# Kernel tuning notes

Hardware: AMD Instinct MI355X
Metric: run time of the kernel (lower is better)

The kernel has to match this reference:

```python
import jax, jax.numpy as jnp
import numpy as np

L, D, H, F, E, K = 2, 512, 8, 2048, 8, 2
V, B, S, T, PAD = 32000, 2, 1024, 1024, 0


def _pe(n, d):
    pos = jnp.arange(n, dtype=jnp.float32)[:, None]
    div = jnp.exp(jnp.arange(0, d, 2, dtype=jnp.float32) * (-np.log(10000.0) / d))
    pe = jnp.zeros((n, d), jnp.float32)
    pe = pe.at[:, 0::2].set(jnp.sin(pos * div)).at[:, 1::2].set(jnp.cos(pos * div))
    return pe


def _ln(x, g, b):
    m = x.mean(-1, keepdims=True)
    v = ((x - m) ** 2).mean(-1, keepdims=True)
    return (x - m) / jnp.sqrt(v + 1e-5) * g + b


def _mha(q_in, k_in, v_in, w, b, mask):
    # w: [4,D,D] (q,k,v,out), b: [4,D]; mask broadcastable to [B,H,Sq,Sk] (True=keep)
    Bq, Sq, Dm = q_in.shape
    Sk = k_in.shape[1]
    dk = Dm // H
    q = (q_in @ w[0] + b[0]).reshape(Bq, Sq, H, dk).transpose(0, 2, 1, 3)
    k = (k_in @ w[1] + b[1]).reshape(Bq, Sk, H, dk).transpose(0, 2, 1, 3)
    v = (v_in @ w[2] + b[2]).reshape(Bq, Sk, H, dk).transpose(0, 2, 1, 3)
    s = jnp.einsum('bhqd,bhkd->bhqk', q, k) / np.sqrt(dk).astype(np.float32)
    s = jnp.where(mask, s, jnp.float32(-1e9))
    a = jax.nn.softmax(s, axis=-1)
    c = jnp.einsum('bhqk,bhkd->bhqd', a, v).transpose(0, 2, 1, 3).reshape(Bq, Sq, Dm)
    return c @ w[3] + b[3]


def _moe(x, gw, gb, w1, b1, w2, b2):
    # token-choice top-k routing with softmax gate probs (no renormalization)
    Bx, Sx, Dm = x.shape
    N = Bx * Sx
    xf = x.reshape(N, Dm)
    probs = jax.nn.softmax(xf @ gw + gb, axis=-1)              # [N,E]
    topv, topi = jax.lax.top_k(probs, K)                        # [N,K]
    comb = jnp.zeros_like(probs).at[jnp.arange(N)[:, None], topi].set(topv)  # [N,E] sparse combine weights
    h = jax.nn.relu(jnp.einsum('nd,edf->nef', xf, w1) + b1)     # [N,E,F]
    eo = jnp.einsum('nef,efd->ned', h, w2) + b2                 # [N,E,D]
    y = jnp.einsum('ne,ned->nd', comb, eo)
    return y.reshape(Bx, Sx, Dm)


def setup_inputs():
    key = jax.random.key(0)
    ks = iter(jax.random.split(key, 32))
    sd, sf = 1.0 / np.sqrt(D), 1.0 / np.sqrt(F)

    def nrm(shape, scale):
        return jax.random.normal(next(ks), shape, jnp.float32) * np.float32(scale)

    inp = {}
    inp['src'] = jax.random.randint(next(ks), (B, S), 0, V)
    inp['tgt'] = jax.random.randint(next(ks), (B, T), 0, V)
    inp['enc_emb'] = nrm((V, D), 0.02).at[PAD].set(0.0)
    inp['dec_emb'] = nrm((V, D), 0.02).at[PAD].set(0.0)
    inp['enc_attn_w'] = nrm((L, 4, D, D), sd)
    inp['enc_attn_b'] = jnp.zeros((L, 4, D), jnp.float32)
    inp['enc_ln_g'] = jnp.ones((L, 2, D), jnp.float32)
    inp['enc_ln_b'] = jnp.zeros((L, 2, D), jnp.float32)
    inp['enc_gate_w'] = nrm((L, D, E), sd)
    inp['enc_gate_b'] = jnp.zeros((L, E), jnp.float32)
    inp['enc_w1'] = nrm((L, E, D, F), sd)
    inp['enc_b1'] = jnp.zeros((L, E, F), jnp.float32)
    inp['enc_w2'] = nrm((L, E, F, D), sf)
    inp['enc_b2'] = jnp.zeros((L, E, D), jnp.float32)
    inp['dec_sa_w'] = nrm((L, 4, D, D), sd)
    inp['dec_sa_b'] = jnp.zeros((L, 4, D), jnp.float32)
    inp['dec_ca_w'] = nrm((L, 4, D, D), sd)
    inp['dec_ca_b'] = jnp.zeros((L, 4, D), jnp.float32)
    inp['dec_ln_g'] = jnp.ones((L, 3, D), jnp.float32)
    inp['dec_ln_b'] = jnp.zeros((L, 3, D), jnp.float32)
    inp['dec_gate_w'] = nrm((L, D, E), sd)
    inp['dec_gate_b'] = jnp.zeros((L, E), jnp.float32)
    inp['dec_w1'] = nrm((L, E, D, F), sd)
    inp['dec_b1'] = jnp.zeros((L, E, F), jnp.float32)
    inp['dec_w2'] = nrm((L, E, F, D), sf)
    inp['dec_b2'] = jnp.zeros((L, E, D), jnp.float32)
    inp['out_w'] = nrm((D, V), sd)
    inp['out_b'] = jnp.zeros((V,), jnp.float32)
    return inp


def reference(src, tgt, enc_emb, dec_emb, enc_attn_w, enc_attn_b, enc_ln_g, enc_ln_b,
              enc_gate_w, enc_gate_b, enc_w1, enc_b1, enc_w2, enc_b2,
              dec_sa_w, dec_sa_b, dec_ca_w, dec_ca_b, dec_ln_g, dec_ln_b,
              dec_gate_w, dec_gate_b, dec_w1, dec_b1, dec_w2, dec_b2, out_w, out_b):
    src_mask = (src != PAD)[:, None, None, :]                                  # [B,1,1,S]
    causal = jnp.tril(jnp.ones((T, T), bool))
    tgt_mask = (tgt != PAD)[:, None, None, :] & causal[None, None]             # [B,1,T,T]

    x = enc_emb[src] + _pe(S, D)[None]                                         # dropout = identity (eval)
    for l in range(L):
        a = _mha(x, x, x, enc_attn_w[l], enc_attn_b[l], src_mask)
        x = _ln(x + a, enc_ln_g[l, 0], enc_ln_b[l, 0])
        f = _moe(x, enc_gate_w[l], enc_gate_b[l], enc_w1[l], enc_b1[l], enc_w2[l], enc_b2[l])
        x = _ln(x + f, enc_ln_g[l, 1], enc_ln_b[l, 1])
    enc_out = x

    y = dec_emb[tgt] + _pe(T, D)[None]
    for l in range(L):
        a = _mha(y, y, y, dec_sa_w[l], dec_sa_b[l], tgt_mask)
        y = _ln(y + a, dec_ln_g[l, 0], dec_ln_b[l, 0])
        c = _mha(y, enc_out, enc_out, dec_ca_w[l], dec_ca_b[l], src_mask)
        y = _ln(y + c, dec_ln_g[l, 1], dec_ln_b[l, 1])
        f = _moe(y, dec_gate_w[l], dec_gate_b[l], dec_w1[l], dec_b1[l], dec_w2[l], dec_b2[l])
        y = _ln(y + f, dec_ln_g[l, 2], dec_ln_b[l, 2])

    return y @ out_w + out_b                                                    # [B,T,V]
```

## Files before the change

### kernel.cpp

```cpp
#include <hip/hip_runtime.h>
#include <hip/hip_bf16.h>

#define L_ 2
#define D_ 512
#define H_ 8
#define DK_ 64
#define F_ 2048
#define E_ 8
#define V_ 32000
#define B_ 2
#define S_ 1024
#define T_ 1024
#define NTOK (B_*S_)
#define MAXPAD 4608
#define RB64   72
#define QLD 1536

typedef unsigned short u16;
typedef _Float16 f16x8 __attribute__((ext_vector_type(8)));
typedef _Float16 f16x4 __attribute__((ext_vector_type(4)));
typedef float f32x4 __attribute__((ext_vector_type(4)));

__device__ __forceinline__ void gload16(const void* g, const void* l) {
    __builtin_amdgcn_global_load_lds(
        (const __attribute__((address_space(1))) void*)g,
        (__attribute__((address_space(3))) void*)l, 16, 0, 0);
}

__device__ __forceinline__ void split_f16(float v, _Float16& h, _Float16& l) {
    h = (_Float16)v;
    l = (_Float16)(v - (float)h);
}

__global__ __launch_bounds__(256) void embed_pe(const int* __restrict__ toks,
                                                const float* __restrict__ emb,
                                                _Float16* __restrict__ oh,
                                                _Float16* __restrict__ ol, int Slen)
{
    int n = blockIdx.x;
    int spos = n % Slen;
    int tok = toks[n];
    const float* erow = emb + (size_t)tok * D_;
    size_t rb = (size_t)n * D_;
    for (int j = threadIdx.x; j < D_; j += 256) {
        int i = j >> 1;
        float arg = (float)spos * expf(-(float)i * 0.035977892f);
        float pe = (j & 1) ? cosf(arg) : sinf(arg);
        float v = erow[j] + pe;
        _Float16 h, l; split_f16(v, h, l);
        oh[rb + j] = h; ol[rb + j] = l;
    }
}

template<bool WLO>
__global__ __launch_bounds__(256) void transpose_w(const float* __restrict__ in,
                                                   _Float16* __restrict__ oh,
                                                   _Float16* __restrict__ ol, int R, int C)
{
    __shared__ float t[64][65];
    size_t sb = (size_t)blockIdx.z * R * C;
    in += sb; oh += sb; if (WLO) ol += sb;
    int c0 = blockIdx.x * 64, r0 = blockIdx.y * 64;
    int tid = threadIdx.x;
    {
        int r = tid >> 4;
        int cq = (tid & 15) * 4;
        #pragma unroll
        for (int p = 0; p < 4; ++p) {
            int rr = r + p * 16;
            float4 v = *(const float4*)&in[(size_t)(r0 + rr) * C + c0 + cq];
            t[rr][cq] = v.x; t[rr][cq + 1] = v.y; t[rr][cq + 2] = v.z; t[rr][cq + 3] = v.w;
        }
    }
    __syncthreads();
    int rp = (tid & 15) * 4;
    int cb = tid >> 4;
    #pragma unroll
    for (int p = 0; p < 4; ++p) {
        int c = cb + p * 16;
        f16x4 hv, lv;
        #pragma unroll
        for (int j = 0; j < 4; ++j) {
            float v = t[rp + j][c];
            _Float16 h = (_Float16)v;
            hv[j] = h;
            if (WLO) lv[j] = (_Float16)(v - (float)h);
        }
        *(f16x4*)&oh[(size_t)(c0 + c) * R + r0 + rp] = hv;
        if (WLO) *(f16x4*)&ol[(size_t)(c0 + c) * R + r0 + rp] = lv;
    }
}

template<int MODE, bool RELU, int OUTMODE, int PASSES, int TM, int TN>
__global__ __launch_bounds__(256, 2) void gemm_mfma(
    const _Float16* __restrict__ Ah, const _Float16* __restrict__ Al,
    const _Float16* __restrict__ Wh, const _Float16* __restrict__ Wl,
    const float* __restrict__ biasbase,
    float* __restrict__ Cf, _Float16* __restrict__ Ch, _Float16* __restrict__ Cl,
    _Float16* __restrict__ vt_h, _Float16* __restrict__ vt_l, int cbase,
    int M, int Kd, int N, int ldc,
    const int* __restrict__ route_tok, const int* __restrict__ rb_expert,
    const int* __restrict__ pad_base, const int* __restrict__ counts)
{
    constexpr int AR = TM / 32;
    constexpr int BR = TN / 32;
    int row0 = blockIdx.x * TM;
    const _Float16* Wmh = Wh;
    const _Float16* Wml = Wl;
    const float* bias = biasbase;
    int vend = M;
    if (MODE != 0) {
        int total = pad_base[E_];
        if (row0 >= total) return;
        int e = rb_expert[row0 >> 6];
        vend = pad_base[e] + counts[e];
        Wmh = Wh + (size_t)e * Kd * N;
        if (PASSES == 3) Wml = Wl + (size_t)e * Kd * N;
        bias = biasbase + (size_t)e * N;
    }
    int col0 = blockIdx.y * TN;
    int tid = threadIdx.x;
    int lane = tid & 63, w = tid >> 6;
    int wm = w >> 1, wn = w & 1;

    __shared__ _Float16 lds[(PASSES == 3 ? 2 : 1) * (TM + TN) * 64];
    _Float16* lAh = lds;
    _Float16* lBh = lds + TM * 64;
    _Float16* lAl = (PASSES == 3) ? lds + (TM + TN) * 64 : nullptr;
    _Float16* lBl = (PASSES == 3) ? lds + (TM + TN) * 64 + TM * 64 : nullptr;

    int srow8 = lane >> 3;
    int q8 = lane & 7;
    size_t aoff[AR], boff[BR];
    #pragma unroll
    for (int j = 0; j < AR; ++j) {
        int m = w * (TM / 4) + j * 8 + srow8;
        int gr = row0 + m;
        int ar = (MODE == 1) ? route_tok[gr] : gr;
        int ss = (q8 ^ (m & 7)) << 3;
        aoff[j] = (size_t)ar * Kd + ss;
    }
    #pragma unroll
    for (int j = 0; j < BR; ++j) {
        int m = w * (TN / 4) + j * 8 + srow8;
        int ss = (q8 ^ (m & 7)) << 3;
        boff[j] = (size_t)(col0 + m) * Kd + ss;
    }

    f32x4 zero4 = {0.f, 0.f, 0.f, 0.f};
    f32x4 acc[AR][BR];
    #pragma unroll
    for (int i = 0; i < AR; ++i)
        #pragma unroll
        for (int j = 0; j < BR; ++j) acc[i][j] = zero4;

    int lm = lane & 15, kg = lane >> 4;

    for (int k0 = 0; k0 < Kd; k0 += 64) {
        #pragma unroll
        for (int j = 0; j < AR; ++j) {
            int lb = (w * (TM / 4) + j * 8) * 64;
            gload16(Ah + aoff[j] + k0, lAh + lb);
            if (PASSES == 3) gload16(Al + aoff[j] + k0, lAl + lb);
        }
        #pragma unroll
        for (int j = 0; j < BR; ++j) {
            int lb = (w * (TN / 4) + j * 8) * 64;
            gload16(Wmh + boff[j] + k0, lBh + lb);
            if (PASSES == 3) gload16(Wml + boff[j] + k0, lBl + lb);
        }
        __syncthreads();
        #pragma unroll
        for (int ks = 0; ks < 2; ++ks) {
            f16x8 ah[AR], bh[BR];
            #pragma unroll
            for (int i = 0; i < AR; ++i) {
                int m = wm * (TM / 2) + i * 16 + lm;
                ah[i] = *(const f16x8*)&lAh[m * 64 + ((((ks << 2) + kg) ^ (m & 7)) << 3)];
            }
            #pragma unroll
            for (int j = 0; j < BR; ++j) {
                int n = wn * (TN / 2) + j * 16 + lm;
                bh[j] = *(const f16x8*)&lBh[n * 64 + ((((ks << 2) + kg) ^ (n & 7)) << 3)];
            }
            #pragma unroll
            for (int i = 0; i < AR; ++i)
                #pragma unroll
                for (int jn = 0; jn < BR; ++jn)
                    acc[i][jn] = __builtin_amdgcn_mfma_f32_16x16x32_f16(ah[i], bh[jn], acc[i][jn], 0, 0, 0);
            if (PASSES == 3) {
                f16x8 bl[BR];
                #pragma unroll
                for (int j = 0; j < BR; ++j) {
                    int n = wn * (TN / 2) + j * 16 + lm;
                    bl[j] = *(const f16x8*)&lBl[n * 64 + ((((ks << 2) + kg) ^ (n & 7)) << 3)];
                }
                #pragma unroll
                for (int i = 0; i < AR; ++i)
                    #pragma unroll
                    for (int jn = 0; jn < BR; ++jn)
                        acc[i][jn] = __builtin_amdgcn_mfma_f32_16x16x32_f16(ah[i], bl[jn], acc[i][jn], 0, 0, 0);
                f16x8 al[AR];
                #pragma unroll
                for (int i = 0; i < AR; ++i) {
                    int m = wm * (TM / 2) + i * 16 + lm;
                    al[i] = *(const f16x8*)&lAl[m * 64 + ((((ks << 2) + kg) ^ (m & 7)) << 3)];
                }
                #pragma unroll
                for (int i = 0; i < AR; ++i)
                    #pragma unroll
                    for (int jn = 0; jn < BR; ++jn)
                        acc[i][jn] = __builtin_amdgcn_mfma_f32_16x16x32_f16(al[i], bh[jn], acc[i][jn], 0, 0, 0);
            }
        }
        __syncthreads();
    }

    float bv[BR];
    #pragma unroll
    for (int jn = 0; jn < BR; ++jn) bv[jn] = bias[col0 + wn * (TN / 2) + jn * 16 + lm];
    int rowb = row0 + wm * (TM / 2) + (lane >> 4) * 4;

    if (OUTMODE == 2 && (col0 + cbase) >= 1024) {
        #pragma unroll
        for (int i = 0; i < AR; ++i) {
            int row = rowb + i * 16;
            int b = row >> 10, q = row & 1023;
            #pragma unroll
            for (int jn = 0; jn < BR; ++jn) {
                int vcol = col0 + cbase - 1024 + wn * (TN / 2) + jn * 16 + lm;
                int hh = vcol >> 6, dd = vcol & 63;
                f16x4 hv, lv;
                #pragma unroll
                for (int r = 0; r < 4; ++r) {
                    float v = acc[i][jn][r] + bv[jn];
                    _Float16 x1, x2; split_f16(v, x1, x2);
                    hv[r] = x1; lv[r] = x2;
                }
                size_t vtoff = ((size_t)((b << 3) + hh) * 64 + dd) * 1024 + q;
                *(f16x4*)&vt_h[vtoff] = hv;
                *(f16x4*)&vt_l[vtoff] = lv;
            }
        }
        return;
    }

    #pragma unroll
    for (int i = 0; i < AR; ++i) {
        #pragma unroll
        for (int r = 0; r < 4; ++r) {
            int row = rowb + i * 16 + r;
            if (MODE != 0 && row >= vend) continue;
            #pragma unroll
            for (int jn = 0; jn < BR; ++jn) {
                float v = acc[i][jn][r] + bv[jn];
                if (RELU) v = fmaxf(v, 0.f);
                int c = col0 + wn * (TN / 2) + jn * 16 + lm;
                if (OUTMODE == 0) {
                    Cf[(size_t)row * ldc + c] = v;
                } else {
                    _Float16 h, l; split_f16(v, h, l);
                    Ch[(size_t)row * ldc + cbase + c] = h;
                    Cl[(size_t)row * ldc + cbase + c] = l;
                }
            }
        }
    }
}

template<int CAUSAL>
__global__ __launch_bounds__(512, 1) void attn_flash(
    const _Float16* __restrict__ qkvh, const _Float16* __restrict__ qkvl,
    const _Float16* __restrict__ vth, const _Float16* __restrict__ vtl,
    const int* __restrict__ ktoks,
    _Float16* __restrict__ ch, _Float16* __restrict__ cl)
{
    int q0 = blockIdx.x * 64;
    int bh = blockIdx.y, b = bh >> 3, h = bh & 7;
    int tid = threadIdx.x, lane = tid & 63, w = tid >> 6;
    int qg = w & 3, kh = w >> 2;
    int lm = lane & 15, kg = lane >> 4;
    int srow8 = lane >> 3, q8 = lane & 7;
    int tb = b * S_;

    __shared__ _Float16 smem[49152];
    _Float16* hb  = smem + kh * 16384;
    _Float16* lKh = hb;
    _Float16* lKl = hb + 4096;
    _Float16* lVh = hb + 8192;
    _Float16* lVl = hb + 12288;
    _Float16* lPh = smem + 32768 + w * 1024;
    _Float16* lPl = smem + 40960 + w * 1024;

    size_t qbase = (size_t)b * S_ * QLD + h * DK_;
    const _Float16* Qh = qkvh + qbase;
    const _Float16* Ql = qkvl + qbase;
    const _Float16* Kh = qkvh + qbase + 512;
    const _Float16* Kl = qkvl + qbase + 512;
    const _Float16* Vh = vth + (size_t)bh * 64 * 1024;
    const _Float16* Vl = vtl + (size_t)bh * 64 * 1024;

    f16x8 qfh[2], qfl[2];
    {
        int qr = q0 + qg * 16 + lm;
        #pragma unroll
        for (int ks = 0; ks < 2; ++ks) {
            qfh[ks] = *(const f16x8*)&Qh[(size_t)qr * QLD + ks * 32 + kg * 8];
            qfl[ks] = *(const f16x8*)&Ql[(size_t)qr * QLD + ks * 32 + kg * 8];
        }
    }

    float mreg[4], lreg[4];
    f32x4 od[4];
    f32x4 zero4 = {0.f, 0.f, 0.f, 0.f};
    #pragma unroll
    for (int r = 0; r < 4; ++r) { mreg[r] = -1e30f; lreg[r] = 0.f; }
    #pragma unroll
    for (int jn = 0; jn < 4; ++jn) od[jn] = zero4;

    int qrow[4];
    #pragma unroll
    for (int r = 0; r < 4; ++r) qrow[r] = q0 + qg * 16 + (lane >> 4) * 4 + r;

    int nkt = CAUSAL ? (q0 >> 6) + 1 : 16;
    int nhalf = (nkt + 1) >> 1;

    for (int it = 0; it < nhalf; ++it) {
        int kt = 2 * it + kh;
        bool active = kt < nkt;
        int k0 = kt * 64;

        if (active) {
            #pragma unroll
            for (int j = 0; j < 2; ++j) {
                int row = qg * 16 + j * 8 + srow8;
                int lb = (qg * 16 + j * 8) * 64;
                int ss = (q8 ^ (row & 7)) << 3;
                gload16(Kh + (size_t)(k0 + row) * QLD + ss, lKh + lb);
                gload16(Kl + (size_t)(k0 + row) * QLD + ss, lKl + lb);
                gload16(Vh + (size_t)row * 1024 + k0 + ss, lVh + lb);
                gload16(Vl + (size_t)row * 1024 + k0 + ss, lVl + lb);
            }
        }
        __syncthreads();

        if (active) {
            bool diag = CAUSAL && (kt == (q0 >> 6));
            f32x4 accs[4];
            #pragma unroll
            for (int jn = 0; jn < 4; ++jn) accs[jn] = zero4;
            #pragma unroll
            for (int ks = 0; ks < 2; ++ks) {
                #pragma unroll
                for (int jn = 0; jn < 4; ++jn) {
                    int n = jn * 16 + lm;
                    int koff = n * 64 + ((((ks << 2) + kg) ^ (n & 7)) << 3);
                    f16x8 bhv = *(const f16x8*)&lKh[koff];
                    f16x8 blv = *(const f16x8*)&lKl[koff];
                    accs[jn] = __builtin_amdgcn_mfma_f32_16x16x32_f16(qfh[ks], bhv, accs[jn], 0, 0, 0);
                    accs[jn] = __builtin_amdgcn_mfma_f32_16x16x32_f16(qfh[ks], blv, accs[jn], 0, 0, 0);
                    accs[jn] = __builtin_amdgcn_mfma_f32_16x16x32_f16(qfl[ks], bhv, accs[jn], 0, 0, 0);
                }
            }

            float sv[4][4];
            #pragma unroll
            for (int jn = 0; jn < 4; ++jn) {
                int kglob = k0 + jn * 16 + lm;
                bool pad_ok = (ktoks[tb + kglob] != 0);
                #pragma unroll
                for (int r = 0; r < 4; ++r) {
                    float s = accs[jn][r] * 0.125f;
                    bool keep = pad_ok && (!diag || kglob <= qrow[r]);
                    sv[jn][r] = keep ? s : -1e9f;
                }
            }
            float pv[4][4];
            #pragma unroll
            for (int r = 0; r < 4; ++r) {
                float tm = fmaxf(fmaxf(sv[0][r], sv[1][r]), fmaxf(sv[2][r], sv[3][r]));
                tm = fmaxf(tm, __shfl_xor(tm, 1));
                tm = fmaxf(tm, __shfl_xor(tm, 2));
                tm = fmaxf(tm, __shfl_xor(tm, 4));
                tm = fmaxf(tm, __shfl_xor(tm, 8));
                float mnew = fmaxf(mreg[r], tm);
                float corr = expf(mreg[r] - mnew);
                lreg[r] *= corr;
                #pragma unroll
                for (int jn = 0; jn < 4; ++jn) od[jn][r] *= corr;
                float psum = 0.f;
                #pragma unroll
                for (int jn = 0; jn < 4; ++jn) {
                    float p = expf(sv[jn][r] - mnew);
                    pv[jn][r] = p;
                    psum += p;
                }
                psum += __shfl_xor(psum, 1);
                psum += __shfl_xor(psum, 2);
                psum += __shfl_xor(psum, 4);
                psum += __shfl_xor(psum, 8);
                lreg[r] += psum;
                mreg[r] = mnew;
            }

            #pragma unroll
            for (int jn = 0; jn < 4; ++jn) {
                int col = jn * 16 + lm;
                #pragma unroll
                for (int r = 0; r < 4; ++r) {
                    int rr = (lane >> 4) * 4 + r;
                    int idx = rr * 64 + (((col >> 3) ^ (rr & 7)) << 3) + (col & 7);
                    _Float16 hh, ll; split_f16(pv[jn][r], hh, ll);
                    lPh[idx] = hh; lPl[idx] = ll;
                }
            }

            #pragma unroll
            for (int ks = 0; ks < 2; ++ks) {
                int poff = lm * 64 + ((((ks << 2) + kg) ^ (lm & 7)) << 3);
                f16x8 pah = *(const f16x8*)&lPh[poff];
                f16x8 pal = *(const f16x8*)&lPl[poff];
                #pragma unroll
                for (int jn = 0; jn < 4; ++jn) {
                    int n = jn * 16 + lm;
                    int noff = n * 64 + ((((ks << 2) + kg) ^ (n & 7)) << 3);
                    f16x8 vbh = *(const f16x8*)&lVh[noff];
                    f16x8 vbl = *(const f16x8*)&lVl[noff];
                    od[jn] = __builtin_amdgcn_mfma_f32_16x16x32_f16(pah, vbh, od[jn], 0, 0, 0);
                    od[jn] = __builtin_amdgcn_mfma_f32_16x16x32_f16(pah, vbl, od[jn], 0, 0, 0);
                    od[jn] = __builtin_amdgcn_mfma_f32_16x16x32_f16(pal, vbh, od[jn], 0, 0, 0);
                }
            }
        }
        __syncthreads();
    }

    float* mrg = (float*)(smem + 32768);
    if (kh == 1) {
        float* mp = mrg + ((size_t)qg * 64 + lane) * 24;
        #pragma unroll
        for (int jn = 0; jn < 4; ++jn)
            #pragma unroll
            for (int r = 0; r < 4; ++r) mp[jn * 4 + r] = od[jn][r];
        #pragma unroll
        for (int r = 0; r < 4; ++r) { mp[16 + r] = mreg[r]; mp[20 + r] = lreg[r]; }
    }
    __syncthreads();
    if (kh == 0) {
        float* mp = mrg + ((size_t)qg * 64 + lane) * 24;
        #pragma unroll
        for (int r = 0; r < 4; ++r) {
            float m1 = mp[16 + r], l1 = mp[20 + r];
            float m = fmaxf(mreg[r], m1);
            float c0 = expf(mreg[r] - m), c1 = expf(m1 - m);
            float inv = 1.0f / (lreg[r] * c0 + l1 * c1);
            size_t rbase = (size_t)(tb + qrow[r]) * D_ + h * DK_;
            #pragma unroll
            for (int jn = 0; jn < 4; ++jn) {
                float o = (od[jn][r] * c0 + mp[jn * 4 + r] * c1) * inv;
                _Float16 hh, ll; split_f16(o, hh, ll);
                int d = jn * 16 + lm;
                ch[rbase + d] = hh; cl[rbase + d] = ll;
            }
        }
    }
}

template<bool GATE>
__global__ __launch_bounds__(256) void ln_add(const _Float16* __restrict__ xh,
                                              const _Float16* __restrict__ xl,
                                              const float* __restrict__ r,
                                              const float* __restrict__ g,
                                              const float* __restrict__ be,
                                              _Float16* __restrict__ oh,
                                              _Float16* __restrict__ ol,
                                              const float* __restrict__ gw,
                                              const float* __restrict__ gb,
                                              float* __restrict__ lg)
{
    int row = blockIdx.x;
    size_t rb = (size_t)row * D_;
    int tid = threadIdx.x;
    float v0 = (float)xh[rb + tid] + (float)xl[rb + tid] + r[rb + tid];
    float v1 = (float)xh[rb + tid + 256] + (float)xl[rb + tid + 256] + r[rb + tid + 256];
    float s = v0 + v1;
    for (int off = 32; off; off >>= 1) s += __shfl_down(s, off);
    __shared__ float red[8];
    __shared__ float gred[4][E_];
    int lane = tid & 63, wid = tid >> 6;
    if (!lane) red[wid] = s;
    __syncthreads();
    if (!tid) red[4] = (red[0] + red[1] + red[2] + red[3]) * (1.0f / 512.0f);
    __syncthreads();
    float m = red[4];
    float d0 = v0 - m, d1 = v1 - m;
    s = d0 * d0 + d1 * d1;
    for (int off = 32; off; off >>= 1) s += __shfl_down(s, off);
    if (!lane) red[wid] = s;
    __syncthreads();
    if (!tid) red[5] = rsqrtf((red[0] + red[1] + red[2] + red[3]) * (1.0f / 512.0f) + 1e-5f);
    __syncthreads();
    float rstd = red[5];
    float y0 = d0 * rstd * g[tid] + be[tid];
    float y1 = d1 * rstd * g[tid + 256] + be[tid + 256];
    _Float16 h, l;
    split_f16(y0, h, l); oh[rb + tid] = h; ol[rb + tid] = l;
    split_f16(y1, h, l); oh[rb + tid + 256] = h; ol[rb + tid + 256] = l;
    if (GATE) {
        float acc[E_];
        const float* g0 = gw + (size_t)tid * E_;
        const float* g1 = gw + (size_t)(tid + 256) * E_;
        #pragma unroll
        for (int e = 0; e < E_; ++e) acc[e] = y0 * g0[e] + y1 * g1[e];
        #pragma unroll
        for (int e = 0; e < E_; ++e)
            for (int off = 32; off; off >>= 1) acc[e] += __shfl_down(acc[e], off);
        if (!lane) {
            #pragma unroll
            for (int e = 0; e < E_; ++e) gred[wid][e] = acc[e];
        }
        __syncthreads();
        if (tid < E_)
            lg[(size_t)row * E_ + tid] = gred[0][tid] + gred[1][tid] + gred[2][tid] + gred[3][tid] + gb[tid];
    }
}

__global__ __launch_bounds__(256) void ln_add_moe(const _Float16* __restrict__ xh,
                                                  const _Float16* __restrict__ xl,
                                                  const float* __restrict__ eo,
                                                  const float* __restrict__ topv,
                                                  const int* __restrict__ route_row,
                                                  const float* __restrict__ g,
                                                  const float* __restrict__ be,
                                                  _Float16* __restrict__ oh,
                                                  _Float16* __restrict__ ol)
{
    int row = blockIdx.x;
    int r0 = route_row[row * 2], r1 = route_row[row * 2 + 1];
    float w0 = topv[row * 2], w1 = topv[row * 2 + 1];
    size_t rb = (size_t)row * D_;
    const float* e0 = eo + (size_t)r0 * D_;
    const float* e1 = eo + (size_t)r1 * D_;
    int tid = threadIdx.x;
    float v0 = (float)xh[rb + tid] + (float)xl[rb + tid] + w0 * e0[tid] + w1 * e1[tid];
    float v1 = (float)xh[rb + tid + 256] + (float)xl[rb + tid + 256] + w0 * e0[tid + 256] + w1 * e1[tid + 256];
    float s = v0 + v1;
    for (int off = 32; off; off >>= 1) s += __shfl_down(s, off);
    __shared__ float red[8];
    int lane = tid & 63, wid = tid >> 6;
    if (!lane) red[wid] = s;
    __syncthreads();
    if (!tid) red[4] = (red[0] + red[1] + red[2] + red[3]) * (1.0f / 512.0f);
    __syncthreads();
    float m = red[4];
    float d0 = v0 - m, d1 = v1 - m;
    s = d0 * d0 + d1 * d1;
    for (int off = 32; off; off >>= 1) s += __shfl_down(s, off);
    if (!lane) red[wid] = s;
    __syncthreads();
    if (!tid) red[5] = rsqrtf((red[0] + red[1] + red[2] + red[3]) * (1.0f / 512.0f) + 1e-5f);
    __syncthreads();
    float rstd = red[5];
    float y0 = d0 * rstd * g[tid] + be[tid];
    float y1 = d1 * rstd * g[tid + 256] + be[tid + 256];
    _Float16 h, l;
    split_f16(y0, h, l); oh[rb + tid] = h; ol[rb + tid] = l;
    split_f16(y1, h, l); oh[rb + tid + 256] = h; ol[rb + tid + 256] = l;
}

__global__ __launch_bounds__(1024) void gate_top2_routes(const float* __restrict__ lg,
                                                         float* __restrict__ topv,
                                                         int* __restrict__ route_tok,
                                                         int* __restrict__ route_row,
                                                         int* __restrict__ counts,
                                                         int* __restrict__ pad_base,
                                                         int* __restrict__ rb_expert)
{
    __shared__ int eid[NTOK * 2];
    __shared__ unsigned short chist[256][8];
    __shared__ int pb[E_ + 1];
    __shared__ int cnt[E_];
    int t = threadIdx.x;
    #pragma unroll
    for (int s2 = 0; s2 < 2; ++s2) {
        int n = t * 2 + s2;
        float l0[E_], p[E_];
        float m = -1e30f;
        #pragma unroll
        for (int e = 0; e < E_; ++e) { l0[e] = lg[n * E_ + e]; m = fmaxf(m, l0[e]); }
        float su = 0.f;
        #pragma unroll
        for (int e = 0; e < E_; ++e) { p[e] = expf(l0[e] - m); su += p[e]; }
        float inv = 1.0f / su;
        int i1 = 0; float v1 = p[0];
        #pragma unroll
        for (int e = 1; e < E_; ++e) if (p[e] > v1) { v1 = p[e]; i1 = e; }
        int i2 = -1; float v2 = -1.f;
        #pragma unroll
        for (int e = 0; e < E_; ++e) if (e != i1 && p[e] > v2) { v2 = p[e]; i2 = e; }
        topv[n * 2] = v1 * inv; topv[n * 2 + 1] = v2 * inv;
        eid[n * 2] = i1; eid[n * 2 + 1] = i2;
    }
    #pragma unroll
    for (int g = 0; g < 5; ++g) route_tok[t + 1024 * g] = 0;
    __syncthreads();

    if (t < 256) {
        int r[16];
        #pragma unroll
        for (int i = 0; i < 16; ++i) r[i] = eid[t * 16 + i];
        #pragma unroll
        for (int e = 0; e < 8; ++e) {
            int h = 0;
            #pragma unroll
            for (int i = 0; i < 16; ++i) h += (r[i] == e) ? 1 : 0;
            chist[t][e] = (unsigned short)h;
        }
    }
    __syncthreads();

    if (t < 8) {
        int run = 0;
        for (int c = 0; c < 256; ++c) {
            int v = chist[c][t];
            chist[c][t] = (unsigned short)run;
            run += v;
        }
        cnt[t] = run;
        counts[t] = run;
    }
    __syncthreads();

    if (t == 0) {
        int pad = 0;
        for (int e = 0; e < 8; ++e) {
            pb[e] = pad;
            pad_base[e] = pad;
            int nb = (cnt[e] + 63) >> 6;
            for (int rb = 0; rb < nb; ++rb) rb_expert[(pad >> 6) + rb] = e;
            pad += nb << 6;
        }
        pb[8] = pad;
        pad_base[8] = pad;
    }
    __syncthreads();

    if (t < 256) {
        int r[16];
        #pragma unroll
        for (int i = 0; i < 16; ++i) r[i] = eid[t * 16 + i];
        #pragma unroll
        for (int e = 0; e < 8; ++e) {
            int o = pb[e] + chist[t][e];
            #pragma unroll
            for (int i = 0; i < 16; ++i) {
                if (r[i] == e) {
                    int slot = t * 16 + i;
                    route_tok[o] = slot >> 1;
                    route_row[slot] = o;
                    o++;
                }
            }
        }
    }
}

extern "C" void kernel_launch(void* const* d_in, const int* in_sizes, int n_in,
                              void* d_out, int out_size, void* d_ws, size_t ws_size,
                              hipStream_t stream)
{
    const int*   src        = (const int*)  d_in[0];
    const int*   tgt        = (const int*)  d_in[1];
    const float* enc_emb    = (const float*)d_in[2];
    const float* dec_emb    = (const float*)d_in[3];
    const float* enc_attn_w = (const float*)d_in[4];
    const float* enc_attn_b = (const float*)d_in[5];
    const float* enc_ln_g   = (const float*)d_in[6];
    const float* enc_ln_b   = (const float*)d_in[7];
    const float* enc_gate_w = (const float*)d_in[8];
    const float* enc_gate_b = (const float*)d_in[9];
    const float* enc_w1     = (const float*)d_in[10];
    const float* enc_b1     = (const float*)d_in[11];
    const float* enc_w2     = (const float*)d_in[12];
    const float* enc_b2     = (const float*)d_in[13];
    const float* dec_sa_w   = (const float*)d_in[14];
    const float* dec_sa_b   = (const float*)d_in[15];
    const float* dec_ca_w   = (const float*)d_in[16];
    const float* dec_ca_b   = (const float*)d_in[17];
    const float* dec_ln_g   = (const float*)d_in[18];
    const float* dec_ln_b   = (const float*)d_in[19];
    const float* dec_gate_w = (const float*)d_in[20];
    const float* dec_gate_b = (const float*)d_in[21];
    const float* dec_w1     = (const float*)d_in[22];
    const float* dec_b1     = (const float*)d_in[23];
    const float* dec_w2     = (const float*)d_in[24];
    const float* dec_b2     = (const float*)d_in[25];
    const float* out_w      = (const float*)d_in[26];
    const float* out_b      = (const float*)d_in[27];
    float* out = (float*)d_out;

    char* ob = (char*)d_out;
    size_t oc = 0;
    auto dalloc = [&](size_t bytes) { char* p = ob + oc; oc += (bytes + 255) & ~(size_t)255; return p; };
    _Float16* qkv_h  = (_Float16*)dalloc((size_t)NTOK * QLD * 2);
    _Float16* qkv_l  = (_Float16*)dalloc((size_t)NTOK * QLD * 2);
    _Float16* vt_h   = (_Float16*)dalloc((size_t)16 * 64 * 1024 * 2);
    _Float16* vt_l   = (_Float16*)dalloc((size_t)16 * 64 * 1024 * 2);
    float* aout  = (float*)dalloc((size_t)NTOK * D_ * 4);
    _Float16* ctx_h = (_Float16*)dalloc((size_t)NTOK * D_ * 2);
    _Float16* ctx_l = (_Float16*)dalloc((size_t)NTOK * D_ * 2);
    _Float16* encA_h = (_Float16*)dalloc((size_t)L_ * 4 * D_ * D_ * 2);
    _Float16* encA_l = (_Float16*)dalloc((size_t)L_ * 4 * D_ * D_ * 2);
    _Float16* saA_h  = (_Float16*)dalloc((size_t)L_ * 4 * D_ * D_ * 2);
    _Float16* saA_l  = (_Float16*)dalloc((size_t)L_ * 4 * D_ * D_ * 2);
    _Float16* caA_h  = (_Float16*)dalloc((size_t)L_ * 4 * D_ * D_ * 2);
    _Float16* caA_l  = (_Float16*)dalloc((size_t)L_ * 4 * D_ * D_ * 2);
    _Float16* xA_h = (_Float16*)dalloc((size_t)NTOK * D_ * 2);
    _Float16* xA_l = (_Float16*)dalloc((size_t)NTOK * D_ * 2);
    _Float16* xB_h = (_Float16*)dalloc((size_t)NTOK * D_ * 2);
    _Float16* xB_l = (_Float16*)dalloc((size_t)NTOK * D_ * 2);
    _Float16* yA_h = (_Float16*)dalloc((size_t)NTOK * D_ * 2);
    _Float16* yA_l = (_Float16*)dalloc((size_t)NTOK * D_ * 2);
    _Float16* yB_h = (_Float16*)dalloc((size_t)NTOK * D_ * 2);
    _Float16* yB_l = (_Float16*)dalloc((size_t)NTOK * D_ * 2);

    char* wp = (char*)d_ws;
    size_t wc = 0;
    auto walloc = [&](size_t bytes) { char* p = wp + wc; wc += (bytes + 255) & ~(size_t)255; return p; };
    _Float16* outwT_h = (_Float16*)walloc((size_t)V_ * D_ * 2);
    _Float16* final_h = (_Float16*)walloc((size_t)NTOK * D_ * 2);
    size_t wsz = (size_t)L_ * E_ * D_ * F_;
    _Float16* ew1t_h = (_Float16*)walloc(wsz * 2);
    _Float16* ew1t_l = (_Float16*)walloc(wsz * 2);
    _Float16* ew2t_h = (_Float16*)walloc(wsz * 2);
    _Float16* ew2t_l = (_Float16*)walloc(wsz * 2);
    _Float16* dw1t_h = (_Float16*)walloc(wsz * 2);
    _Float16* dw1t_l = (_Float16*)walloc(wsz * 2);
    _Float16* dw2t_h = (_Float16*)walloc(wsz * 2);
    _Float16* dw2t_l = (_Float16*)walloc(wsz * 2);
    _Float16* hbuf_h  = (_Float16*)walloc((size_t)MAXPAD * F_ * 2);
    _Float16* hbuf_l  = (_Float16*)walloc((size_t)MAXPAD * F_ * 2);
    float*    eobuf   = (float*)walloc((size_t)MAXPAD * D_ * 4);
    float* lg   = (float*)walloc((size_t)NTOK * E_ * 4);
    float* topv = (float*)walloc((size_t)NTOK * 2 * 4);
    int*   route_tok = (int*)walloc((size_t)5120 * 4);
    int*   route_row = (int*)walloc((size_t)NTOK * 2 * 4);
    int*   counts    = (int*)walloc(64);
    int*   pad_base  = (int*)walloc(64);
    int*   rb_expert = (int*)walloc((size_t)128 * 4);

    transpose_w<true><<<dim3(8, 8, 8), 256, 0, stream>>>(enc_attn_w, encA_h, encA_l, D_, D_);
    transpose_w<true><<<dim3(8, 8, 8), 256, 0, stream>>>(dec_sa_w, saA_h, saA_l, D_, D_);
    transpose_w<true><<<dim3(8, 8, 8), 256, 0, stream>>>(dec_ca_w, caA_h, caA_l, D_, D_);
    transpose_w<false><<<dim3(500, 8, 1), 256, 0, stream>>>(out_w, outwT_h, nullptr, D_, V_);
    transpose_w<true><<<dim3(32, 8, L_ * E_), 256, 0, stream>>>(enc_w1, ew1t_h, ew1t_l, D_, F_);
    transpose_w<true><<<dim3(8, 32, L_ * E_), 256, 0, stream>>>(enc_w2, ew2t_h, ew2t_l, F_, D_);
    transpose_w<true><<<dim3(32, 8, L_ * E_), 256, 0, stream>>>(dec_w1, dw1t_h, dw1t_l, D_, F_);
    transpose_w<true><<<dim3(8, 32, L_ * E_), 256, 0, stream>>>(dec_w2, dw2t_h, dw2t_l, F_, D_);

    auto run_mha = [&](const _Float16* q_h, const _Float16* q_l,
                       const _Float16* kv_h, const _Float16* kv_l,
                       const _Float16* wT_h, const _Float16* wT_l, const float* bt,
                       const int* ktoks, int causal, bool fused) {
        if (fused) {
            gemm_mfma<0, false, 2, 3, 64, 128><<<dim3(32, 12), 256, 0, stream>>>(
                q_h, q_l, wT_h, wT_l, bt, nullptr, qkv_h, qkv_l, vt_h, vt_l, 0,
                NTOK, D_, 1536, QLD, nullptr, nullptr, nullptr, nullptr);
        } else {
            gemm_mfma<0, false, 1, 3, 64, 64><<<dim3(32, 8), 256, 0, stream>>>(
                q_h, q_l, wT_h, wT_l, bt, nullptr, qkv_h, qkv_l, nullptr, nullptr, 0,
                NTOK, D_, 512, QLD, nullptr, nullptr, nullptr, nullptr);
            gemm_mfma<0, false, 2, 3, 64, 128><<<dim3(32, 8), 256, 0, stream>>>(
                kv_h, kv_l, wT_h + (size_t)D_ * D_, wT_l + (size_t)D_ * D_, bt + D_,
                nullptr, qkv_h, qkv_l, vt_h, vt_l, 512,
                NTOK, D_, 1024, QLD, nullptr, nullptr, nullptr, nullptr);
        }
        if (causal)
            attn_flash<1><<<dim3(16, 16), 512, 0, stream>>>(qkv_h, qkv_l, vt_h, vt_l, ktoks, ctx_h, ctx_l);
        else
            attn_flash<0><<<dim3(16, 16), 512, 0, stream>>>(qkv_h, qkv_l, vt_h, vt_l, ktoks, ctx_h, ctx_l);
        gemm_mfma<0, false, 0, 3, 64, 64><<<dim3(32, 8), 256, 0, stream>>>(
            ctx_h, ctx_l, wT_h + (size_t)3 * D_ * D_, wT_l + (size_t)3 * D_ * D_,
            bt + 3 * D_, aout, nullptr, nullptr, nullptr, nullptr, 0,
            NTOK, D_, 512, 512, nullptr, nullptr, nullptr, nullptr);
    };

    auto run_moe = [&](const _Float16* x_h, const _Float16* x_l,
                       const _Float16* w1h, const _Float16* w1l,
                       const _Float16* w2h, const _Float16* w2l,
                       const float* b1p, const float* b2p, bool p3) {
        gate_top2_routes<<<1, 1024, 0, stream>>>(lg, topv, route_tok, route_row, counts, pad_base, rb_expert);
        if (p3) {
            gemm_mfma<1, true, 1, 3, 64, 128><<<dim3(RB64, 16), 256, 0, stream>>>(
                x_h, x_l, w1h, w1l, b1p, nullptr, hbuf_h, hbuf_l, nullptr, nullptr, 0,
                0, D_, F_, F_, route_tok, rb_expert, pad_base, counts);
            gemm_mfma<2, false, 0, 3, 64, 64><<<dim3(RB64, 8), 256, 0, stream>>>(
                hbuf_h, hbuf_l, w2h, w2l, b2p, eobuf, nullptr, nullptr, nullptr, nullptr, 0,
                0, F_, D_, D_, route_tok, rb_expert, pad_base, counts);
        } else {
            gemm_mfma<1, true, 1, 1, 64, 128><<<dim3(RB64, 16), 256, 0, stream>>>(
                x_h, nullptr, w1h, nullptr, b1p, nullptr, hbuf_h, hbuf_l, nullptr, nullptr, 0,
                0, D_, F_, F_, route_tok, rb_expert, pad_base, counts);
            gemm_mfma<2, false, 0, 1, 64, 64><<<dim3(RB64, 8), 256, 0, stream>>>(
                hbuf_h, nullptr, w2h, nullptr, b2p, eobuf, nullptr, nullptr, nullptr, nullptr, 0,
                0, F_, D_, D_, route_tok, rb_expert, pad_base, counts);
        }
    };

    embed_pe<<<B_ * S_, 256, 0, stream>>>(src, enc_emb, xA_h, xA_l, S_);
    _Float16* cur_h = xA_h; _Float16* cur_l = xA_l;
    _Float16* alt_h = xB_h; _Float16* alt_l = xB_l;
    for (int l = 0; l < L_; ++l) {
        run_mha(cur_h, cur_l, nullptr, nullptr,
                encA_h + (size_t)l * 4 * D_ * D_, encA_l + (size_t)l * 4 * D_ * D_,
                enc_attn_b + (size_t)l * 4 * D_, src, 0, true);
        ln_add<true><<<NTOK, 256, 0, stream>>>(cur_h, cur_l, aout,
            enc_ln_g + (size_t)(l * 2 + 0) * D_, enc_ln_b + (size_t)(l * 2 + 0) * D_,
            alt_h, alt_l, enc_gate_w + (size_t)l * D_ * E_, enc_gate_b + (size_t)l * E_, lg);
        { _Float16* t = cur_h; cur_h = alt_h; alt_h = t; t = cur_l; cur_l = alt_l; alt_l = t; }
        run_moe(cur_h, cur_l,
                ew1t_h + (size_t)l * E_ * D_ * F_, ew1t_l + (size_t)l * E_ * D_ * F_,
                ew2t_h + (size_t)l * E_ * D_ * F_, ew2t_l + (size_t)l * E_ * D_ * F_,
                enc_b1 + (size_t)l * E_ * F_, enc_b2 + (size_t)l * E_ * D_, true);
        ln_add_moe<<<NTOK, 256, 0, stream>>>(cur_h, cur_l, eobuf, topv, route_row,
            enc_ln_g + (size_t)(l * 2 + 1) * D_, enc_ln_b + (size_t)(l * 2 + 1) * D_,
            alt_h, alt_l);
        { _Float16* t = cur_h; cur_h = alt_h; alt_h = t; t = cur_l; cur_l = alt_l; alt_l = t; }
    }
    _Float16* enc_h = cur_h; _Float16* enc_l = cur_l;

    embed_pe<<<B_ * T_, 256, 0, stream>>>(tgt, dec_emb, yA_h, yA_l, T_);
    _Float16* dc_h = yA_h; _Float16* dc_l = yA_l;
    _Float16* da_h = yB_h; _Float16* da_l = yB_l;
    for (int l = 0; l < L_; ++l) {
        run_mha(dc_h, dc_l, nullptr, nullptr,
                saA_h + (size_t)l * 4 * D_ * D_, saA_l + (size_t)l * 4 * D_ * D_,
                dec_sa_b + (size_t)l * 4 * D_, tgt, 1, true);
        ln_add<false><<<NTOK, 256, 0, stream>>>(dc_h, dc_l, aout,
            dec_ln_g + (size_t)(l * 3 + 0) * D_, dec_ln_b + (size_t)(l * 3 + 0) * D_,
            da_h, da_l, nullptr, nullptr, nullptr);
        { _Float16* t = dc_h; dc_h = da_h; da_h = t; t = dc_l; dc_l = da_l; da_l = t; }
        run_mha(dc_h, dc_l, enc_h, enc_l,
                caA_h + (size_t)l * 4 * D_ * D_, caA_l + (size_t)l * 4 * D_ * D_,
                dec_ca_b + (size_t)l * 4 * D_, src, 0, false);
        ln_add<true><<<NTOK, 256, 0, stream>>>(dc_h, dc_l, aout,
            dec_ln_g + (size_t)(l * 3 + 1) * D_, dec_ln_b + (size_t)(l * 3 + 1) * D_,
            da_h, da_l, dec_gate_w + (size_t)l * D_ * E_, dec_gate_b + (size_t)l * E_, lg);
        { _Float16* t = dc_h; dc_h = da_h; da_h = t; t = dc_l; dc_l = da_l; da_l = t; }
        bool last = (l == L_ - 1);
        run_moe(dc_h, dc_l,
                dw1t_h + (size_t)l * E_ * D_ * F_, dw1t_l + (size_t)l * E_ * D_ * F_,
                dw2t_h + (size_t)l * E_ * D_ * F_, dw2t_l + (size_t)l * E_ * D_ * F_,
                dec_b1 + (size_t)l * E_ * F_, dec_b2 + (size_t)l * E_ * D_, !last);
        ln_add_moe<<<NTOK, 256, 0, stream>>>(dc_h, dc_l, eobuf, topv, route_row,
            dec_ln_g + (size_t)(l * 3 + 2) * D_, dec_ln_b + (size_t)(l * 3 + 2) * D_,
            last ? final_h : da_h, da_l);
        { _Float16* t = dc_h; dc_h = da_h; da_h = t; t = dc_l; dc_l = da_l; da_l = t; }
    }

    gemm_mfma<0, false, 0, 1, 128, 128><<<dim3(NTOK / 128, V_ / 128), 256, 0, stream>>>(
        final_h, nullptr, outwT_h, nullptr, out_b, out, nullptr, nullptr, nullptr, nullptr, 0,
        NTOK, D_, V_, V_, nullptr, nullptr, nullptr, nullptr);
}
```

Before: 1.224 ms.

## Use 128-row MoE expert tiles, swizzle vocab GEMM grid, parallelize routing scan

Expert GEMMs switch from 64-row to 128-row tiles, so routing pads each expert to 128 rows and uses a larger padded buffer. This gives more weight reuse per block but adds padding waste. The output vocab GEMM gets a block-index swizzle meant to improve cache locality. The serial per-expert prefix scan in routing becomes a two-level parallel scan, and the three attention weight transposes are merged into one launch to cut launch overhead.

```diff
diff --git a/kernel.cpp b/kernel.cpp
--- a/kernel.cpp
+++ b/kernel.cpp
@@ -12,8 +12,8 @@
 #define S_ 1024
 #define T_ 1024
 #define NTOK (B_*S_)
-#define MAXPAD 4608
-#define RB64   72
+#define MAXPAD 5120
+#define RBLK   40
 #define QLD 1536
 
 typedef unsigned short u16;
@@ -91,7 +91,50 @@
     }
 }
 
-template<int MODE, bool RELU, int OUTMODE, int PASSES, int TM, int TN>
+__global__ __launch_bounds__(256) void transpose_w3(
+    const float* __restrict__ i0, _Float16* __restrict__ h0, _Float16* __restrict__ l0,
+    const float* __restrict__ i1, _Float16* __restrict__ h1, _Float16* __restrict__ l1,
+    const float* __restrict__ i2, _Float16* __restrict__ h2, _Float16* __restrict__ l2)
+{
+    __shared__ float t[64][65];
+    int set = blockIdx.z >> 3, sub = blockIdx.z & 7;
+    const float* in = (set == 0) ? i0 : (set == 1) ? i1 : i2;
+    _Float16* oh = (set == 0) ? h0 : (set == 1) ? h1 : h2;
+    _Float16* ol = (set == 0) ? l0 : (set == 1) ? l1 : l2;
+    size_t sb = (size_t)sub * D_ * D_;
+    in += sb; oh += sb; ol += sb;
+    int c0 = blockIdx.x * 64, r0 = blockIdx.y * 64;
+    int tid = threadIdx.x;
+    {
+        int r = tid >> 4;
+        int cq = (tid & 15) * 4;
+        #pragma unroll
+        for (int p = 0; p < 4; ++p) {
+            int rr = r + p * 16;
+            float4 v = *(const float4*)&in[(size_t)(r0 + rr) * D_ + c0 + cq];
+            t[rr][cq] = v.x; t[rr][cq + 1] = v.y; t[rr][cq + 2] = v.z; t[rr][cq + 3] = v.w;
+        }
+    }
+    __syncthreads();
+    int rp = (tid & 15) * 4;
+    int cb = tid >> 4;
+    #pragma unroll
+    for (int p = 0; p < 4; ++p) {
+        int c = cb + p * 16;
+        f16x4 hv, lv;
+        #pragma unroll
+        for (int j = 0; j < 4; ++j) {
+            float v = t[rp + j][c];
+            _Float16 h = (_Float16)v;
+            hv[j] = h;
+            lv[j] = (_Float16)(v - (float)h);
+        }
+        *(f16x4*)&oh[(size_t)(c0 + c) * D_ + r0 + rp] = hv;
+        *(f16x4*)&ol[(size_t)(c0 + c) * D_ + r0 + rp] = lv;
+    }
+}
+
+template<int MODE, bool RELU, int OUTMODE, int PASSES, int TM, int TN, bool SWZ>
 __global__ __launch_bounds__(256, 2) void gemm_mfma(
     const _Float16* __restrict__ Ah, const _Float16* __restrict__ Al,
     const _Float16* __restrict__ Wh, const _Float16* __restrict__ Wl,
@@ -104,7 +147,15 @@
 {
     constexpr int AR = TM / 32;
     constexpr int BR = TN / 32;
-    int row0 = blockIdx.x * TM;
+    int bx = blockIdx.x, by = blockIdx.y;
+    if (SWZ) {
+        int total = gridDim.x * gridDim.y;
+        int n = by * gridDim.x + bx;
+        int q = total >> 3;
+        int w2 = (n & 7) * q + (n >> 3);
+        bx = w2 % gridDim.x; by = w2 / gridDim.x;
+    }
+    int row0 = bx * TM;
     const _Float16* Wmh = Wh;
     const _Float16* Wml = Wl;
     const float* bias = biasbase;
@@ -112,13 +163,13 @@
     if (MODE != 0) {
         int total = pad_base[E_];
         if (row0 >= total) return;
-        int e = rb_expert[row0 >> 6];
+        int e = rb_expert[row0 >> 7];
         vend = pad_base[e] + counts[e];
         Wmh = Wh + (size_t)e * Kd * N;
         if (PASSES == 3) Wml = Wl + (size_t)e * Kd * N;
         bias = biasbase + (size_t)e * N;
     }
-    int col0 = blockIdx.y * TN;
+    int col0 = by * TN;
     int tid = threadIdx.x;
     int lane = tid & 63, w = tid >> 6;
     int wm = w >> 1, wn = w & 1;
@@ -578,6 +629,7 @@
 {
     __shared__ int eid[NTOK * 2];
     __shared__ unsigned short chist[256][8];
+    __shared__ unsigned short segb[8][16];
     __shared__ int pb[E_ + 1];
     __shared__ int cnt[E_];
     int t = threadIdx.x;
@@ -619,15 +671,36 @@
     }
     __syncthreads();
 
+    if (t < 128) {
+        int e = t >> 4, seg = t & 15;
+        int s = 0;
+        #pragma unroll
+        for (int i = 0; i < 16; ++i) s += chist[seg * 16 + i][e];
+        segb[e][seg] = (unsigned short)s;
+    }
+    __syncthreads();
     if (t < 8) {
         int run = 0;
-        for (int c = 0; c < 256; ++c) {
-            int v = chist[c][t];
-            chist[c][t] = (unsigned short)run;
+        #pragma unroll
+        for (int sg = 0; sg < 16; ++sg) {
+            int v = segb[t][sg];
+            segb[t][sg] = (unsigned short)run;
             run += v;
         }
         cnt[t] = run;
         counts[t] = run;
+    }
+    __syncthreads();
+    if (t < 128) {
+        int e = t >> 4, seg = t & 15;
+        int run = segb[e][seg];
+        #pragma unroll
+        for (int i = 0; i < 16; ++i) {
+            int c = seg * 16 + i;
+            int v = chist[c][e];
+            chist[c][e] = (unsigned short)run;
+            run += v;
+        }
     }
     __syncthreads();
 
@@ -636,9 +709,9 @@
         for (int e = 0; e < 8; ++e) {
             pb[e] = pad;
             pad_base[e] = pad;
-            int nb = (cnt[e] + 63) >> 6;
-            for (int rb = 0; rb < nb; ++rb) rb_expert[(pad >> 6) + rb] = e;
-            pad += nb << 6;
+            int nb = (cnt[e] + 127) >> 7;
+            for (int rb = 0; rb < nb; ++rb) rb_expert[(pad >> 7) + rb] = e;
+            pad += nb << 7;
         }
         pb[8] = pad;
         pad_base[8] = pad;
@@ -743,15 +816,14 @@
     float*    eobuf   = (float*)walloc((size_t)MAXPAD * D_ * 4);
     float* lg   = (float*)walloc((size_t)NTOK * E_ * 4);
     float* topv = (float*)walloc((size_t)NTOK * 2 * 4);
-    int*   route_tok = (int*)walloc((size_t)5120 * 4);
+    int*   route_tok = (int*)walloc((size_t)MAXPAD * 4);
     int*   route_row = (int*)walloc((size_t)NTOK * 2 * 4);
     int*   counts    = (int*)walloc(64);
     int*   pad_base  = (int*)walloc(64);
     int*   rb_expert = (int*)walloc((size_t)128 * 4);
 
-    transpose_w<true><<<dim3(8, 8, 8), 256, 0, stream>>>(enc_attn_w, encA_h, encA_l, D_, D_);
-    transpose_w<true><<<dim3(8, 8, 8), 256, 0, stream>>>(dec_sa_w, saA_h, saA_l, D_, D_);
-    transpose_w<true><<<dim3(8, 8, 8), 256, 0, stream>>>(dec_ca_w, caA_h, caA_l, D_, D_);
+    transpose_w3<<<dim3(8, 8, 24), 256, 0, stream>>>(
+        enc_attn_w, encA_h, encA_l, dec_sa_w, saA_h, saA_l, dec_ca_w, caA_h, caA_l);
     transpose_w<false><<<dim3(500, 8, 1), 256, 0, stream>>>(out_w, outwT_h, nullptr, D_, V_);
     transpose_w<true><<<dim3(32, 8, L_ * E_), 256, 0, stream>>>(enc_w1, ew1t_h, ew1t_l, D_, F_);
     transpose_w<true><<<dim3(8, 32, L_ * E_), 256, 0, stream>>>(enc_w2, ew2t_h, ew2t_l, F_, D_);
@@ -763,14 +835,14 @@
                        const _Float16* wT_h, const _Float16* wT_l, const float* bt,
                        const int* ktoks, int causal, bool fused) {
         if (fused) {
-            gemm_mfma<0, false, 2, 3, 64, 128><<<dim3(32, 12), 256, 0, stream>>>(
+            gemm_mfma<0, false, 2, 3, 64, 128, false><<<dim3(32, 12), 256, 0, stream>>>(
                 q_h, q_l, wT_h, wT_l, bt, nullptr, qkv_h, qkv_l, vt_h, vt_l, 0,
                 NTOK, D_, 1536, QLD, nullptr, nullptr, nullptr, nullptr);
         } else {
-            gemm_mfma<0, false, 1, 3, 64, 64><<<dim3(32, 8), 256, 0, stream>>>(
+            gemm_mfma<0, false, 1, 3, 64, 64, false><<<dim3(32, 8), 256, 0, stream>>>(
                 q_h, q_l, wT_h, wT_l, bt, nullptr, qkv_h, qkv_l, nullptr, nullptr, 0,
                 NTOK, D_, 512, QLD, nullptr, nullptr, nullptr, nullptr);
-            gemm_mfma<0, false, 2, 3, 64, 128><<<dim3(32, 8), 256, 0, stream>>>(
+            gemm_mfma<0, false, 2, 3, 64, 128, false><<<dim3(32, 8), 256, 0, stream>>>(
                 kv_h, kv_l, wT_h + (size_t)D_ * D_, wT_l + (size_t)D_ * D_, bt + D_,
                 nullptr, qkv_h, qkv_l, vt_h, vt_l, 512,
                 NTOK, D_, 1024, QLD, nullptr, nullptr, nullptr, nullptr);
@@ -779,7 +851,7 @@
             attn_flash<1><<<dim3(16, 16), 512, 0, stream>>>(qkv_h, qkv_l, vt_h, vt_l, ktoks, ctx_h, ctx_l);
         else
             attn_flash<0><<<dim3(16, 16), 512, 0, stream>>>(qkv_h, qkv_l, vt_h, vt_l, ktoks, ctx_h, ctx_l);
-        gemm_mfma<0, false, 0, 3, 64, 64><<<dim3(32, 8), 256, 0, stream>>>(
+        gemm_mfma<0, false, 0, 3, 64, 64, false><<<dim3(32, 8), 256, 0, stream>>>(
             ctx_h, ctx_l, wT_h + (size_t)3 * D_ * D_, wT_l + (size_t)3 * D_ * D_,
             bt + 3 * D_, aout, nullptr, nullptr, nullptr, nullptr, 0,
             NTOK, D_, 512, 512, nullptr, nullptr, nullptr, nullptr);
@@ -791,17 +863,17 @@
                        const float* b1p, const float* b2p, bool p3) {
         gate_top2_routes<<<1, 1024, 0, stream>>>(lg, topv, route_tok, route_row, counts, pad_base, rb_expert);
         if (p3) {
-            gemm_mfma<1, true, 1, 3, 64, 128><<<dim3(RB64, 16), 256, 0, stream>>>(
+            gemm_mfma<1, true, 1, 3, 128, 128, false><<<dim3(RBLK, 16), 256, 0, stream>>>(
                 x_h, x_l, w1h, w1l, b1p, nullptr, hbuf_h, hbuf_l, nullptr, nullptr, 0,
                 0, D_, F_, F_, route_tok, rb_expert, pad_base, counts);
-            gemm_mfma<2, false, 0, 3, 64, 64><<<dim3(RB64, 8), 256, 0, stream>>>(
+            gemm_mfma<2, false, 0, 3, 128, 64, false><<<dim3(RBLK, 8), 256, 0, stream>>>(
                 hbuf_h, hbuf_l, w2h, w2l, b2p, eobuf, nullptr, nullptr, nullptr, nullptr, 0,
                 0, F_, D_, D_, route_tok, rb_expert, pad_base, counts);
         } else {
-            gemm_mfma<1, true, 1, 1, 64, 128><<<dim3(RB64, 16), 256, 0, stream>>>(
+            gemm_mfma<1, true, 1, 1, 128, 128, false><<<dim3(RBLK, 16), 256, 0, stream>>>(
                 x_h, nullptr, w1h, nullptr, b1p, nullptr, hbuf_h, hbuf_l, nullptr, nullptr, 0,
                 0, D_, F_, F_, route_tok, rb_expert, pad_base, counts);
-            gemm_mfma<2, false, 0, 1, 64, 64><<<dim3(RB64, 8), 256, 0, stream>>>(
+            gemm_mfma<2, false, 0, 1, 128, 64, false><<<dim3(RBLK, 8), 256, 0, stream>>>(
                 hbuf_h, nullptr, w2h, nullptr, b2p, eobuf, nullptr, nullptr, nullptr, nullptr, 0,
                 0, F_, D_, D_, route_tok, rb_expert, pad_base, counts);
         }
@@ -858,7 +930,7 @@
         { _Float16* t = dc_h; dc_h = da_h; da_h = t; t = dc_l; dc_l = da_l; da_l = t; }
     }
 
-    gemm_mfma<0, false, 0, 1, 128, 128><<<dim3(NTOK / 128, V_ / 128), 256, 0, stream>>>(
+    gemm_mfma<0, false, 0, 1, 128, 128, true><<<dim3(NTOK / 128, V_ / 128), 256, 0, stream>>>(
         final_h, nullptr, outwT_h, nullptr, out_b, out, nullptr, nullptr, nullptr, nullptr, 0,
         NTOK, D_, V_, V_, nullptr, nullptr, nullptr, nullptr);
 }
```

New measurement: 1.251 ms. +2.2%, slower.
